# Kernel optimization log

Hardware: AMD Instinct MI355X
Metric: run time of the kernel (lower is better)

Reference implementation:

```python
import jax, jax.numpy as jnp
import numpy as np

N, E, D, K, NCONV = 50000, 800000, 64, 3, 6


def setup_inputs() -> dict:
    key = jax.random.key(0)
    ks = jax.random.split(key, 6)
    X = jax.random.normal(ks[0], (N, D), jnp.float32)
    edge_index = jax.random.randint(ks[1], (2, E), 0, N, dtype=jnp.int64)
    edge_weight = jax.random.uniform(ks[2], (E,), jnp.float32)
    H = jax.random.normal(ks[3], (N, D), jnp.float32)
    lambda_max = jnp.ones((1,), jnp.float32) * 2.0  # typical sym-normalized Laplacian bound
    conv_w = jax.random.normal(ks[4], (NCONV, K, D, D), jnp.float32) / np.sqrt(D)
    conv_b = jnp.zeros((NCONV, D), jnp.float32)
    return {"X": X, "edge_index": edge_index, "edge_weight": edge_weight,
            "H": H, "lambda_max": lambda_max, "conv_w": conv_w, "conv_b": conv_b}


def reference(X, edge_index, edge_weight, H, lambda_max, conv_w, conv_b):
    src, dst = edge_index[0], edge_index[1]
    # symmetric normalization: norm_e = w_e / sqrt(deg_src * deg_dst)
    deg = jax.ops.segment_sum(edge_weight, src, num_segments=N)
    dinv = jnp.where(deg > 0, deg ** -0.5, 0.0)
    norm = edge_weight * dinv[src] * dinv[dst]  # [E]
    lam = lambda_max.reshape(())
    c = 2.0 / lam

    def a_prop(v):  # A_norm @ v via scatter-add over edges, [N,D]
        return jax.ops.segment_sum(norm[:, None] * v[src], dst, num_segments=N)

    def l_hat(v):  # (2/lam)(I - A_norm) v - v
        return (c - 1.0) * v - c * a_prop(v)

    def cheb(v, w, b):  # ChebConv order K: sum_k T_k(L_hat) v @ W_k + b
        tx0, tx1 = v, l_hat(v)
        out = tx0 @ w[0] + tx1 @ w[1]
        for k in range(2, K):
            tx2 = 2.0 * l_hat(tx1) - tx0
            out = out + tx2 @ w[k]
            tx0, tx1 = tx1, tx2
        return out + b

    Z = jax.nn.sigmoid(cheb(X, conv_w[0], conv_b[0]) + cheb(H, conv_w[1], conv_b[1]))
    R = jax.nn.sigmoid(cheb(X, conv_w[2], conv_b[2]) + cheb(H, conv_w[3], conv_b[3]))
    H_tilde = jnp.tanh(cheb(X, conv_w[4], conv_b[4]) + cheb(H * R, conv_w[5], conv_b[5]))
    return Z * H_tilde + (1.0 - Z) * H
```

## Files before the change

kernel.cpp:

```cpp
#include <hip/hip_runtime.h>
#include <cstdint>
#include <cstddef>

typedef unsigned int u32;
typedef unsigned short u16;
typedef unsigned long long u64;

#define D 64
#define CAP 5120
#define CPAD 16
#define CEMAX 2048

typedef __attribute__((ext_vector_type(8))) short bf16x8;
typedef __attribute__((ext_vector_type(4))) float f32x4;

static __device__ __forceinline__ float sigmoidf_(float x) {
    return 1.f / (1.f + __expf(-x));
}
static __device__ __forceinline__ u16 f2bf(float x) {
    u32 u = __float_as_uint(x);
    return (u16)((u + 0x7fffu + ((u >> 16) & 1u)) >> 16);
}
static __device__ __forceinline__ u32 packbf2(float a, float b) {
    return (u32)f2bf(a) | ((u32)f2bf(b) << 16);
}
static __device__ __forceinline__ float bflo(u32 u) { return __uint_as_float(u << 16); }
static __device__ __forceinline__ float bfhi(u32 u) { return __uint_as_float(u & 0xffff0000u); }


__global__ void init_kernel(u32* cur_d, u32* cur_s) {
    int t = threadIdx.x;
    cur_d[t * CPAD] = (u32)(t * CAP);
    cur_s[t * CPAD] = (u32)(t * CAP);
}

__global__ __launch_bounds__(256) void coarse_prep_kernel(
    const int* __restrict__ src, const int* __restrict__ dst, const float* __restrict__ w,
    u32* cur_d, u32* cur_s,
    u64* __restrict__ slab_d, u32* __restrict__ slab_s,
    const float* __restrict__ X, const float* __restrict__ Hf,
    const float* __restrict__ convw,
    u32* __restrict__ XH_t, u32* __restrict__ WT,
    int E, int CE, int nch, int total) {
    __shared__ __align__(16) char smem[CEMAX * 12 + 6 * 1024];
    int t = threadIdx.x;
    int blk = blockIdx.x;

    if (blk >= nch) {
        int pb = blk - nch;
        if (pb < 18) {
            float (*s)[68] = (float (*)[68])smem;
            const float* wp = convw + (size_t)pb * 4096;
            for (int i = t; i < 1024; i += 256) {
                int k = i >> 4, c4 = (i & 15) * 4;
                *(float4*)&s[k][c4] = *(const float4*)&wp[k * 64 + c4];
            }
            __syncthreads();
            for (int i = t; i < 2048; i += 256) {
                int uk = i & 31, nn = i >> 5;
                WT[(size_t)pb * 2048 + nn * 32 + uk] = packbf2(s[2 * uk][nn], s[2 * uk + 1][nn]);
            }
            return;
        }
        int i = (pb - 18) * 256 + t;
        if (i >= total) return;
        int nn = i >> 6, l = i & 63;
        const float* sp = (l < 32 ? X : Hf) + (size_t)nn * 64 + ((2 * l) & 63);
        float2 v = *(const float2*)sp;
        XH_t[i] = packbf2(v.x, v.y);
        return;
    }

    u64* st_d = (u64*)smem;
    u32* st_s = (u32*)(smem + CEMAX * 8);
    u32* hd = (u32*)(smem + CEMAX * 12);
    u32* hs = hd + 256;
    u32* bd = hs + 256;
    u32* bs = bd + 256;
    u32* gd = bs + 256;
    u32* gs = gd + 256;
    int c = blk;
    hd[t] = 0; hs[t] = 0;
    __syncthreads();
    int e0 = c * CE, e1 = min(E, e0 + CE);
    int m = e1 - e0;
    for (int e = e0 + t; e < e1; e += 256) {
        atomicAdd(&hd[(u32)dst[e] >> 8], 1u);
        atomicAdd(&hs[(u32)src[e] >> 8], 1u);
    }
    __syncthreads();
    u32 vd = hd[t], vs = hs[t];
    bd[t] = vd; bs[t] = vs;
    __syncthreads();
    for (int o = 1; o < 256; o <<= 1) {
        u32 ad = (t >= o) ? bd[t - o] : 0u;
        u32 as = (t >= o) ? bs[t - o] : 0u;
        __syncthreads();
        bd[t] += ad; bs[t] += as;
        __syncthreads();
    }
    u32 exd = bd[t] - vd, exs = bs[t] - vs;
    gd[t] = atomicAdd(&cur_d[t * CPAD], vd);
    gs[t] = atomicAdd(&cur_s[t * CPAD], vs);
    bd[t] = exd; bs[t] = exs;
    hd[t] = exd; hs[t] = exs;
    __syncthreads();
    for (int e = e0 + t; e < e1; e += 256) {
        int s = src[e], d = dst[e];
        float wf = w[e];
        u32 pbd = (u32)d >> 8, pbs = (u32)s >> 8;
        u32 pd = atomicAdd(&hd[pbd], 1u);
        u32 ps = atomicAdd(&hs[pbs], 1u);
        st_d[pd] = (u64)((u32)s | (((u32)d & 255u) << 16) | (pbd << 24)) |
                   ((u64)__float_as_uint(wf) << 32);
        st_s[ps] = ((u32)s & 255u) | (pbs << 8) | ((u32)f2bf(wf) << 16);
    }
    __syncthreads();
    for (int i = t; i < m; i += 256) {
        u64 r = st_d[i];
        u32 b = (u32)(r >> 24) & 255u;
        u32 gpos = gd[b] + ((u32)i - bd[b]);
        if (gpos < (b + 1u) * CAP) slab_d[gpos] = r;
    }
    for (int i = t; i < m; i += 256) {
        u32 r = st_s[i];
        u32 b = (r >> 8) & 255u;
        u32 gpos = gs[b] + ((u32)i - bs[b]);
        if (gpos < (b + 1u) * CAP) slab_s[gpos] = r;
    }
}

__global__ __launch_bounds__(256) void fine_deg_bprefix_kernel(
    const u32* __restrict__ slab_s, const u32* __restrict__ cur_s,
    const u32* __restrict__ cur_d, float* __restrict__ dinv,
    u32* __restrict__ bstart, int NB, int N_) {
    int t = threadIdx.x;
    if ((int)blockIdx.x == NB) {
        __shared__ int sd[256];
        int v = (t < NB) ? min((int)cur_d[t * CPAD] - t * CAP, CAP) : 0;
        sd[t] = v;
        __syncthreads();
        for (int o = 1; o < 256; o <<= 1) {
            int a = (t >= o) ? sd[t - o] : 0;
            __syncthreads();
            sd[t] += a;
            __syncthreads();
        }
        bstart[t] = (u32)(sd[t] - v);
        return;
    }
    __shared__ float dg[256];
    int b = blockIdx.x;
    int m = min((int)cur_s[b * CPAD] - b * CAP, CAP);
    const u32* rp = slab_s + (size_t)b * CAP;
    dg[t] = 0.f;
    __syncthreads();
    for (int i = t; i < m; i += 256) {
        u32 r = rp[i];
        atomicAdd(&dg[r & 255u], __uint_as_float(r & 0xffff0000u));
    }
    __syncthreads();
    int node = (b << 8) + t;
    if (node < N_) dinv[node] = (dg[t] > 0.f) ? rsqrtf(dg[t]) : 0.f;
}

__global__ __launch_bounds__(256) void fine_dst_kernel(
    const u64* __restrict__ slab, const u32* __restrict__ cur_d,
    const u32* __restrict__ bstart, const float* __restrict__ dinv,
    u32* __restrict__ edge4,
    int* __restrict__ cnt, int* __restrict__ row_start, int N_) {
    __shared__ int h[256], sd[256], cur[256];
    int b = blockIdx.x, t = threadIdx.x;
    int m = min((int)cur_d[b * CPAD] - b * CAP, CAP);
    const u64* rp = slab + (size_t)b * CAP;
    h[t] = 0;
    __syncthreads();
    for (int i = t; i < m; i += 256) atomicAdd(&h[(int)((rp[i] >> 16) & 255u)], 1);
    __syncthreads();
    int v = h[t];
    sd[t] = v;
    __syncthreads();
    for (int o = 1; o < 256; o <<= 1) {
        int a = (t >= o) ? sd[t - o] : 0;
        __syncthreads();
        sd[t] += a;
        __syncthreads();
    }
    int excl = sd[t] - v;
    cur[t] = excl;
    int bs = (int)bstart[b];
    int node = (b << 8) + t;
    if (node < N_) { cnt[node] = v; row_start[node] = bs + excl; }
    __syncthreads();
    for (int i = t; i < m; i += 256) {
        u64 r = rp[i];
        int f = (int)((r >> 16) & 255u);
        int p = atomicAdd(&cur[f], 1);
        u32 sidx = (u32)(r & 0xffffu);
        float wf = __uint_as_float((u32)(r >> 32));
        float wn = wf * dinv[sidx];
        edge4[bs + p] = sidx | ((u32)f2bf(wn) << 16);
    }
}


__global__ __launch_bounds__(256) void lhat128_kernel(
    const u32* __restrict__ vt, const u32* __restrict__ w0t,
    u32* __restrict__ out_t,
    const int* __restrict__ rs, const int* __restrict__ cnt, const float* __restrict__ dinv,
    const u32* __restrict__ edges, const float* __restrict__ lam_ptr, int n) {
    int node = (blockIdx.x * blockDim.x + threadIdx.x) >> 6;
    if (node >= n) return;
    int l = threadIdx.x & 63;
    int g = l >> 4, f = l & 15;
    int e0 = rs[node], end = e0 + cnt[node];
    float acc[8];
#pragma unroll
    for (int j = 0; j < 8; j++) acc[j] = 0.f;

    int base = e0;
    for (; base + 16 <= end; base += 16) {
        u32 r0 = edges[base + g];
        u32 r1 = edges[base + 4 + g];
        u32 r2 = edges[base + 8 + g];
        u32 r3 = edges[base + 12 + g];
        const uint4 q0 = *(const uint4*)(vt + (size_t)(r0 & 0xffffu) * 64 + 4 * f);
        const uint4 q1 = *(const uint4*)(vt + (size_t)(r1 & 0xffffu) * 64 + 4 * f);
        const uint4 q2 = *(const uint4*)(vt + (size_t)(r2 & 0xffffu) * 64 + 4 * f);
        const uint4 q3 = *(const uint4*)(vt + (size_t)(r3 & 0xffffu) * 64 + 4 * f);
        float n0 = __uint_as_float(r0 & 0xffff0000u);
        float n1 = __uint_as_float(r1 & 0xffff0000u);
        float n2 = __uint_as_float(r2 & 0xffff0000u);
        float n3 = __uint_as_float(r3 & 0xffff0000u);
        acc[0] += n0 * bflo(q0.x); acc[1] += n0 * bfhi(q0.x);
        acc[2] += n0 * bflo(q0.y); acc[3] += n0 * bfhi(q0.y);
        acc[4] += n0 * bflo(q0.z); acc[5] += n0 * bfhi(q0.z);
        acc[6] += n0 * bflo(q0.w); acc[7] += n0 * bfhi(q0.w);
        acc[0] += n1 * bflo(q1.x); acc[1] += n1 * bfhi(q1.x);
        acc[2] += n1 * bflo(q1.y); acc[3] += n1 * bfhi(q1.y);
        acc[4] += n1 * bflo(q1.z); acc[5] += n1 * bfhi(q1.z);
        acc[6] += n1 * bflo(q1.w); acc[7] += n1 * bfhi(q1.w);
        acc[0] += n2 * bflo(q2.x); acc[1] += n2 * bfhi(q2.x);
        acc[2] += n2 * bflo(q2.y); acc[3] += n2 * bfhi(q2.y);
        acc[4] += n2 * bflo(q2.z); acc[5] += n2 * bfhi(q2.z);
        acc[6] += n2 * bflo(q2.w); acc[7] += n2 * bfhi(q2.w);
        acc[0] += n3 * bflo(q3.x); acc[1] += n3 * bfhi(q3.x);
        acc[2] += n3 * bflo(q3.y); acc[3] += n3 * bfhi(q3.y);
        acc[4] += n3 * bflo(q3.z); acc[5] += n3 * bfhi(q3.z);
        acc[6] += n3 * bflo(q3.w); acc[7] += n3 * bfhi(q3.w);
    }
    for (; base < end; base += 4) {
        int ei = base + g;
        u32 r0 = (ei < end) ? edges[ei] : 0u;
        const uint4 q0 = *(const uint4*)(vt + (size_t)(r0 & 0xffffu) * 64 + 4 * f);
        float n0 = __uint_as_float(r0 & 0xffff0000u);
        acc[0] += n0 * bflo(q0.x); acc[1] += n0 * bfhi(q0.x);
        acc[2] += n0 * bflo(q0.y); acc[3] += n0 * bfhi(q0.y);
        acc[4] += n0 * bflo(q0.z); acc[5] += n0 * bfhi(q0.z);
        acc[6] += n0 * bflo(q0.w); acc[7] += n0 * bfhi(q0.w);
    }
#pragma unroll
    for (int m = 16; m <= 32; m <<= 1)
#pragma unroll
        for (int j = 0; j < 8; j++) acc[j] += __shfl_xor(acc[j], m);

    const uint4 sv = *(const uint4*)(vt + (size_t)node * 64 + 4 * f);
    float self[8];
    self[0] = bflo(sv.x); self[1] = bfhi(sv.x);
    self[2] = bflo(sv.y); self[3] = bfhi(sv.y);
    self[4] = bflo(sv.z); self[5] = bfhi(sv.z);
    self[6] = bflo(sv.w); self[7] = bfhi(sv.w);
    float c = 2.f / lam_ptr[0];
    float dv = dinv[node];
    float rx[8];
#pragma unroll
    for (int j = 0; j < 8; j++) rx[j] = (c - 1.f) * self[j] - (c * dv) * acc[j];
    if (w0t) {
        const uint4 wv4 = *(const uint4*)(w0t + (size_t)node * 64 + 4 * f);
        rx[0] = 2.f * rx[0] - bflo(wv4.x); rx[1] = 2.f * rx[1] - bfhi(wv4.x);
        rx[2] = 2.f * rx[2] - bflo(wv4.y); rx[3] = 2.f * rx[3] - bfhi(wv4.y);
        rx[4] = 2.f * rx[4] - bflo(wv4.z); rx[5] = 2.f * rx[5] - bfhi(wv4.z);
        rx[6] = 2.f * rx[6] - bflo(wv4.w); rx[7] = 2.f * rx[7] - bfhi(wv4.w);
    }
    if (l < 16) {
        uint4 o;
        o.x = packbf2(rx[0], rx[1]); o.y = packbf2(rx[2], rx[3]);
        o.z = packbf2(rx[4], rx[5]); o.w = packbf2(rx[6], rx[7]);
        *(uint4*)(out_t + (size_t)node * 64 + 4 * f) = o;
    }
}

__global__ __launch_bounds__(256) void lhat64_kernel(
    const u32* __restrict__ vt, const u32* __restrict__ w0t,
    u32* __restrict__ out_t,
    const int* __restrict__ rs, const int* __restrict__ cnt, const float* __restrict__ dinv,
    const u32* __restrict__ edges, const float* __restrict__ lam_ptr, int n) {
    int node = (blockIdx.x * blockDim.x + threadIdx.x) >> 6;
    if (node >= n) return;
    int l = threadIdx.x & 63;
    int g = l >> 3, f = l & 7;
    int e0 = rs[node], end = e0 + cnt[node];
    float acc[8];
#pragma unroll
    for (int j = 0; j < 8; j++) acc[j] = 0.f;

    int base = e0;
    for (; base + 16 <= end; base += 16) {
        u32 r0 = edges[base + g];
        u32 r1 = edges[base + 8 + g];
        const uint4 q0 = *(const uint4*)(vt + (size_t)(r0 & 0xffffu) * 32 + 4 * f);
        const uint4 q1 = *(const uint4*)(vt + (size_t)(r1 & 0xffffu) * 32 + 4 * f);
        float n0 = __uint_as_float(r0 & 0xffff0000u);
        float n1 = __uint_as_float(r1 & 0xffff0000u);
        acc[0] += n0 * bflo(q0.x); acc[1] += n0 * bfhi(q0.x);
        acc[2] += n0 * bflo(q0.y); acc[3] += n0 * bfhi(q0.y);
        acc[4] += n0 * bflo(q0.z); acc[5] += n0 * bfhi(q0.z);
        acc[6] += n0 * bflo(q0.w); acc[7] += n0 * bfhi(q0.w);
        acc[0] += n1 * bflo(q1.x); acc[1] += n1 * bfhi(q1.x);
        acc[2] += n1 * bflo(q1.y); acc[3] += n1 * bfhi(q1.y);
        acc[4] += n1 * bflo(q1.z); acc[5] += n1 * bfhi(q1.z);
        acc[6] += n1 * bflo(q1.w); acc[7] += n1 * bfhi(q1.w);
    }
    for (; base < end; base += 8) {
        int ei = base + g;
        u32 r0 = (ei < end) ? edges[ei] : 0u;
        const uint4 q0 = *(const uint4*)(vt + (size_t)(r0 & 0xffffu) * 32 + 4 * f);
        float n0 = __uint_as_float(r0 & 0xffff0000u);
        acc[0] += n0 * bflo(q0.x); acc[1] += n0 * bfhi(q0.x);
        acc[2] += n0 * bflo(q0.y); acc[3] += n0 * bfhi(q0.y);
        acc[4] += n0 * bflo(q0.z); acc[5] += n0 * bfhi(q0.z);
        acc[6] += n0 * bflo(q0.w); acc[7] += n0 * bfhi(q0.w);
    }
#pragma unroll
    for (int m = 8; m <= 32; m <<= 1)
#pragma unroll
        for (int j = 0; j < 8; j++) acc[j] += __shfl_xor(acc[j], m);

    const uint4 sv = *(const uint4*)(vt + (size_t)node * 32 + 4 * f);
    float self[8];
    self[0] = bflo(sv.x); self[1] = bfhi(sv.x);
    self[2] = bflo(sv.y); self[3] = bfhi(sv.y);
    self[4] = bflo(sv.z); self[5] = bfhi(sv.z);
    self[6] = bflo(sv.w); self[7] = bfhi(sv.w);
    float c = 2.f / lam_ptr[0];
    float dv = dinv[node];
    float rx[8];
#pragma unroll
    for (int j = 0; j < 8; j++) rx[j] = (c - 1.f) * self[j] - (c * dv) * acc[j];
    if (w0t) {
        const uint4 wv4 = *(const uint4*)(w0t + (size_t)node * 32 + 4 * f);
        rx[0] = 2.f * rx[0] - bflo(wv4.x); rx[1] = 2.f * rx[1] - bfhi(wv4.x);
        rx[2] = 2.f * rx[2] - bflo(wv4.y); rx[3] = 2.f * rx[3] - bfhi(wv4.y);
        rx[4] = 2.f * rx[4] - bflo(wv4.z); rx[5] = 2.f * rx[5] - bfhi(wv4.z);
        rx[6] = 2.f * rx[6] - bflo(wv4.w); rx[7] = 2.f * rx[7] - bfhi(wv4.w);
    }
    if (l < 8) {
        uint4 o;
        o.x = packbf2(rx[0], rx[1]); o.y = packbf2(rx[2], rx[3]);
        o.z = packbf2(rx[4], rx[5]); o.w = packbf2(rx[6], rx[7]);
        *(uint4*)(out_t + (size_t)node * 32 + 4 * f) = o;
    }
}

__global__ __launch_bounds__(256) void gemm_gate_kernel(
    const u32* __restrict__ A0, const u32* __restrict__ A1, const u32* __restrict__ A2,
    const u32* __restrict__ WT, const float* __restrict__ convb,
    const float* __restrict__ Hf,
    float* __restrict__ Zb, float* __restrict__ Sh,
    u16* __restrict__ HR_t, int n) {
    __shared__ u32 Ws[64 * 36];
    int t = threadIdx.x;
    int wv = t >> 6, l = t & 63;
    int q = l >> 4, ml = l & 15;
    int R = blockIdx.x * 64 + wv * 16;
    int ar = R + ml; if (ar >= n) ar = n - 1;

    f32x4 S[3][4];
#pragma unroll
    for (int tg = 0; tg < 3; tg++)
#pragma unroll
        for (int ni = 0; ni < 4; ni++) S[tg][ni] = (f32x4){0.f, 0.f, 0.f, 0.f};

    for (int kt = 0; kt < 3; kt++) {
        const u32* Ap = (kt == 0) ? A0 : ((kt == 1) ? A1 : A2);
        const u32* ap = Ap + (size_t)ar * 64 + q * 4;
        bf16x8 af[2][2];
        af[0][0] = *(const bf16x8*)(ap +  0);
        af[1][0] = *(const bf16x8*)(ap + 16);
        af[0][1] = *(const bf16x8*)(ap + 32);
        af[1][1] = *(const bf16x8*)(ap + 48);
#pragma unroll
        for (int cg = 0; cg < 5; cg++) {
            int hf = cg & 1, tg = cg >> 1;
            const u32* Wp = WT + (size_t)(cg * 3 + kt) * 2048;
            __syncthreads();
            {
                int i0 = t * 4, i1 = i0 + 1024;
                uint4 w0 = *(const uint4*)(Wp + i0);
                uint4 w1 = *(const uint4*)(Wp + i1);
                *(uint4*)&Ws[(i0 >> 5) * 36 + (i0 & 31)] = w0;
                *(uint4*)&Ws[(i1 >> 5) * 36 + (i1 & 31)] = w1;
            }
            __syncthreads();
#pragma unroll
            for (int h = 0; h < 2; h++) {
                bf16x8 bw[4];
#pragma unroll
                for (int ni = 0; ni < 4; ni++)
                    bw[ni] = *(const bf16x8*)&Ws[(ni * 16 + ml) * 36 + q * 4 + h * 16];
#pragma unroll
                for (int ni = 0; ni < 4; ni++)
                    S[tg][ni] = __builtin_amdgcn_mfma_f32_16x16x32_bf16(
                        af[h][hf], bw[ni], S[tg][ni], 0, 0, 0);
            }
        }
    }
#pragma unroll
    for (int ni = 0; ni < 4; ni++) {
        int col = ni * 16 + ml;
        float bz = convb[col] + convb[64 + col];
        float br = convb[128 + col] + convb[192 + col];
#pragma unroll
        for (int reg = 0; reg < 4; reg++) {
            int row = R + q * 4 + reg;
            if (row < n) {
                size_t o = (size_t)row * 64 + col;
                float z = sigmoidf_(S[0][ni][reg] + bz);
                float r = sigmoidf_(S[1][ni][reg] + br);
                float hr = Hf[o] * r;
                Zb[o] = z;
                Sh[o] = S[2][ni][reg];
                HR_t[o] = f2bf(hr);
            }
        }
    }
}

__global__ __launch_bounds__(256) void gemm_final_kernel(
    const u32* __restrict__ A0, const u32* __restrict__ A1, const u32* __restrict__ A2,
    const u32* __restrict__ WT, const float* __restrict__ convb,
    const float* __restrict__ Zb, const float* __restrict__ Sh, const float* __restrict__ Hf,
    float* __restrict__ outp, int n) {
    __shared__ u32 Ws[64 * 36];
    int t = threadIdx.x;
    int wv = t >> 6, l = t & 63;
    int q = l >> 4, ml = l & 15;
    int R = blockIdx.x * 64 + wv * 16;
    int ar = R + ml; if (ar >= n) ar = n - 1;

    f32x4 S[4];
#pragma unroll
    for (int ni = 0; ni < 4; ni++) S[ni] = (f32x4){0.f, 0.f, 0.f, 0.f};

    for (int kt = 0; kt < 3; kt++) {
        const u32* Ap = (kt == 0) ? A0 : ((kt == 1) ? A1 : A2);
        const u32* ap = Ap + (size_t)ar * 32 + q * 4;
        bf16x8 af[2];
        af[0] = *(const bf16x8*)(ap +  0);
        af[1] = *(const bf16x8*)(ap + 16);
        const u32* Wp = WT + (size_t)(15 + kt) * 2048;
        __syncthreads();
        {
            int i0 = t * 4, i1 = i0 + 1024;
            uint4 w0 = *(const uint4*)(Wp + i0);
            uint4 w1 = *(const uint4*)(Wp + i1);
            *(uint4*)&Ws[(i0 >> 5) * 36 + (i0 & 31)] = w0;
            *(uint4*)&Ws[(i1 >> 5) * 36 + (i1 & 31)] = w1;
        }
        __syncthreads();
#pragma unroll
        for (int h = 0; h < 2; h++) {
            bf16x8 bw[4];
#pragma unroll
            for (int ni = 0; ni < 4; ni++)
                bw[ni] = *(const bf16x8*)&Ws[(ni * 16 + ml) * 36 + q * 4 + h * 16];
#pragma unroll
            for (int ni = 0; ni < 4; ni++)
                S[ni] = __builtin_amdgcn_mfma_f32_16x16x32_bf16(af[h], bw[ni], S[ni], 0, 0, 0);
        }
    }
#pragma unroll
    for (int ni = 0; ni < 4; ni++) {
        int col = ni * 16 + ml;
        float bh = convb[256 + col] + convb[320 + col];
#pragma unroll
        for (int reg = 0; reg < 4; reg++) {
            int row = R + q * 4 + reg;
            if (row < n) {
                size_t o = (size_t)row * 64 + col;
                float z = Zb[o];
                float ht = tanhf(S[ni][reg] + Sh[o] + bh);
                outp[o] = z * ht + (1.f - z) * Hf[o];
            }
        }
    }
}


extern "C" void kernel_launch(void* const* d_in, const int* in_sizes, int n_in,
                              void* d_out, int out_size, void* d_ws, size_t ws_size,
                              hipStream_t stream) {
    const float* X     = (const float*)d_in[0];
    const int*   ei    = (const int*)d_in[1];
    const float* ew    = (const float*)d_in[2];
    const float* H     = (const float*)d_in[3];
    const float* lam   = (const float*)d_in[4];
    const float* convw = (const float*)d_in[5];
    const float* convb = (const float*)d_in[6];
    float* out = (float*)d_out;

    const int N = in_sizes[0] / D;
    const int E = in_sizes[2];
    const int* src = ei;
    const int* dst = ei + E;

    const int NB = (N + 255) >> 8;
    const int nch = (E + CEMAX - 1) / CEMAX;
    const int CE = (E + nch - 1) / nch;

    char* p = (char*)d_ws;
    auto alloc = [&](size_t bytes) {
        void* r = (void*)p;
        p += (bytes + 255) & ~(size_t)255;
        return r;
    };
    float* Zb   = (float*)alloc((size_t)N * 64 * 4);
    float* Sh   = (float*)alloc((size_t)N * 64 * 4);
    u32* XH_t = (u32*)alloc((size_t)N * 64 * 4);
    u32* T1_t = (u32*)alloc((size_t)N * 64 * 4);
    u32* T2_t = (u32*)alloc((size_t)N * 64 * 4);
    u16* HR_t = (u16*)alloc((size_t)N * 64 * 2);
    u16* U1_t = (u16*)alloc((size_t)N * 64 * 2);
    u16* U2_t = (u16*)alloc((size_t)N * 64 * 2);
    u32* edge4 = (u32*)alloc((size_t)E * 4);
    u64* slab_d = (u64*)alloc((size_t)NB * CAP * 8);
    u32* slab_s = (u32*)alloc((size_t)NB * CAP * 4);
    u32* cur_d  = (u32*)alloc(256 * CPAD * 4);
    u32* cur_s  = (u32*)alloc(256 * CPAD * 4);
    u32* bstart = (u32*)alloc(256 * 4);
    int* cnt       = (int*)alloc((size_t)N * 4);
    int* row_start = (int*)alloc((size_t)N * 4);
    float* dinv    = (float*)alloc((size_t)N * 4);
    u32* WT = (u32*)alloc((size_t)18 * 2048 * 4);

    const int BLK = 256;
    const int gND  = (N * D + BLK - 1) / BLK;
    const int gWav = gND;
    const int gx64 = (N + 63) / 64;

    init_kernel<<<1, 256, 0, stream>>>(cur_d, cur_s);
    coarse_prep_kernel<<<nch + 18 + gND, BLK, 0, stream>>>(
        src, dst, ew, cur_d, cur_s, slab_d, slab_s,
        X, H, convw, XH_t, WT, E, CE, nch, N * D);
    fine_deg_bprefix_kernel<<<NB + 1, BLK, 0, stream>>>(slab_s, cur_s, cur_d, dinv, bstart, NB, N);
    fine_dst_kernel<<<NB, BLK, 0, stream>>>(slab_d, cur_d, bstart, dinv, edge4, cnt, row_start, N);

    lhat128_kernel<<<gWav, BLK, 0, stream>>>(XH_t, nullptr, T1_t,
                                             row_start, cnt, dinv, edge4, lam, N);
    lhat128_kernel<<<gWav, BLK, 0, stream>>>(T1_t, XH_t, T2_t,
                                             row_start, cnt, dinv, edge4, lam, N);

    gemm_gate_kernel<<<gx64, BLK, 0, stream>>>(XH_t, T1_t, T2_t, WT, convb, H,
                                               Zb, Sh, HR_t, N);

    lhat64_kernel<<<gWav, BLK, 0, stream>>>((const u32*)HR_t, nullptr, (u32*)U1_t,
                                            row_start, cnt, dinv, edge4, lam, N);
    lhat64_kernel<<<gWav, BLK, 0, stream>>>((const u32*)U1_t, (const u32*)HR_t, (u32*)U2_t,
                                            row_start, cnt, dinv, edge4, lam, N);

    gemm_final_kernel<<<gx64, BLK, 0, stream>>>((const u32*)HR_t, (const u32*)U1_t, (const u32*)U2_t,
                                                WT, convb, Zb, Sh, H, out, N);
}
```

Baseline: 286.8 us.

## Merge fine binning kernels, apply source dinv in SpMM, widen GEMM blocks

```diff
diff --git a/kernel.cpp b/kernel.cpp
--- a/kernel.cpp
+++ b/kernel.cpp
@@ -130,49 +130,32 @@
     }
 }
 
-__global__ __launch_bounds__(256) void fine_deg_bprefix_kernel(
-    const u32* __restrict__ slab_s, const u32* __restrict__ cur_s,
-    const u32* __restrict__ cur_d, float* __restrict__ dinv,
-    u32* __restrict__ bstart, int NB, int N_) {
+__global__ __launch_bounds__(256) void fine_fused_kernel(
+    const u64* __restrict__ slab_d, const u32* __restrict__ slab_s,
+    const u32* __restrict__ cur_d, const u32* __restrict__ cur_s,
+    float* __restrict__ dinv, u32* __restrict__ edge4,
+    int* __restrict__ cnt, int* __restrict__ row_start, int NB, int N_) {
     int t = threadIdx.x;
-    if ((int)blockIdx.x == NB) {
-        __shared__ int sd[256];
-        int v = (t < NB) ? min((int)cur_d[t * CPAD] - t * CAP, CAP) : 0;
-        sd[t] = v;
-        __syncthreads();
-        for (int o = 1; o < 256; o <<= 1) {
-            int a = (t >= o) ? sd[t - o] : 0;
-            __syncthreads();
-            sd[t] += a;
-            __syncthreads();
-        }
-        bstart[t] = (u32)(sd[t] - v);
+    int b = blockIdx.x;
+    if (b < NB) {
+        __shared__ float dg[256];
+        int m = min((int)cur_s[b * CPAD] - b * CAP, CAP);
+        const u32* rp = slab_s + (size_t)b * CAP;
+        dg[t] = 0.f;
+        __syncthreads();
+        for (int i = t; i < m; i += 256) {
+            u32 r = rp[i];
+            atomicAdd(&dg[r & 255u], __uint_as_float(r & 0xffff0000u));
+        }
+        __syncthreads();
+        int node = (b << 8) + t;
+        if (node < N_) dinv[node] = (dg[t] > 0.f) ? rsqrtf(dg[t]) : 0.f;
         return;
     }
-    __shared__ float dg[256];
-    int b = blockIdx.x;
-    int m = min((int)cur_s[b * CPAD] - b * CAP, CAP);
-    const u32* rp = slab_s + (size_t)b * CAP;
-    dg[t] = 0.f;
-    __syncthreads();
-    for (int i = t; i < m; i += 256) {
-        u32 r = rp[i];
-        atomicAdd(&dg[r & 255u], __uint_as_float(r & 0xffff0000u));
-    }
-    __syncthreads();
-    int node = (b << 8) + t;
-    if (node < N_) dinv[node] = (dg[t] > 0.f) ? rsqrtf(dg[t]) : 0.f;
-}
-
-__global__ __launch_bounds__(256) void fine_dst_kernel(
-    const u64* __restrict__ slab, const u32* __restrict__ cur_d,
-    const u32* __restrict__ bstart, const float* __restrict__ dinv,
-    u32* __restrict__ edge4,
-    int* __restrict__ cnt, int* __restrict__ row_start, int N_) {
+    b -= NB;
     __shared__ int h[256], sd[256], cur[256];
-    int b = blockIdx.x, t = threadIdx.x;
     int m = min((int)cur_d[b * CPAD] - b * CAP, CAP);
-    const u64* rp = slab + (size_t)b * CAP;
+    const u64* rp = slab_d + (size_t)b * CAP;
     h[t] = 0;
     __syncthreads();
     for (int i = t; i < m; i += 256) atomicAdd(&h[(int)((rp[i] >> 16) & 255u)], 1);
@@ -188,7 +171,7 @@
     }
     int excl = sd[t] - v;
     cur[t] = excl;
-    int bs = (int)bstart[b];
+    int bs = b * CAP;
     int node = (b << 8) + t;
     if (node < N_) { cnt[node] = v; row_start[node] = bs + excl; }
     __syncthreads();
@@ -198,8 +181,7 @@
         int p = atomicAdd(&cur[f], 1);
         u32 sidx = (u32)(r & 0xffffu);
         float wf = __uint_as_float((u32)(r >> 32));
-        float wn = wf * dinv[sidx];
-        edge4[bs + p] = sidx | ((u32)f2bf(wn) << 16);
+        edge4[bs + p] = sidx | ((u32)f2bf(wf) << 16);
     }
 }
 
@@ -224,14 +206,18 @@
         u32 r1 = edges[base + 4 + g];
         u32 r2 = edges[base + 8 + g];
         u32 r3 = edges[base + 12 + g];
+        float d0 = dinv[r0 & 0xffffu];
+        float d1 = dinv[r1 & 0xffffu];
+        float d2 = dinv[r2 & 0xffffu];
+        float d3 = dinv[r3 & 0xffffu];
         const uint4 q0 = *(const uint4*)(vt + (size_t)(r0 & 0xffffu) * 64 + 4 * f);
         const uint4 q1 = *(const uint4*)(vt + (size_t)(r1 & 0xffffu) * 64 + 4 * f);
         const uint4 q2 = *(const uint4*)(vt + (size_t)(r2 & 0xffffu) * 64 + 4 * f);
         const uint4 q3 = *(const uint4*)(vt + (size_t)(r3 & 0xffffu) * 64 + 4 * f);
-        float n0 = __uint_as_float(r0 & 0xffff0000u);
-        float n1 = __uint_as_float(r1 & 0xffff0000u);
-        float n2 = __uint_as_float(r2 & 0xffff0000u);
-        float n3 = __uint_as_float(r3 & 0xffff0000u);
+        float n0 = __uint_as_float(r0 & 0xffff0000u) * d0;
+        float n1 = __uint_as_float(r1 & 0xffff0000u) * d1;
+        float n2 = __uint_as_float(r2 & 0xffff0000u) * d2;
+        float n3 = __uint_as_float(r3 & 0xffff0000u) * d3;
         acc[0] += n0 * bflo(q0.x); acc[1] += n0 * bfhi(q0.x);
         acc[2] += n0 * bflo(q0.y); acc[3] += n0 * bfhi(q0.y);
         acc[4] += n0 * bflo(q0.z); acc[5] += n0 * bfhi(q0.z);
@@ -252,8 +238,9 @@
     for (; base < end; base += 4) {
         int ei = base + g;
         u32 r0 = (ei < end) ? edges[ei] : 0u;
+        float d0 = dinv[r0 & 0xffffu];
         const uint4 q0 = *(const uint4*)(vt + (size_t)(r0 & 0xffffu) * 64 + 4 * f);
-        float n0 = __uint_as_float(r0 & 0xffff0000u);
+        float n0 = __uint_as_float(r0 & 0xffff0000u) * d0;
         acc[0] += n0 * bflo(q0.x); acc[1] += n0 * bfhi(q0.x);
         acc[2] += n0 * bflo(q0.y); acc[3] += n0 * bfhi(q0.y);
         acc[4] += n0 * bflo(q0.z); acc[5] += n0 * bfhi(q0.z);
@@ -308,10 +295,12 @@
     for (; base + 16 <= end; base += 16) {
         u32 r0 = edges[base + g];
         u32 r1 = edges[base + 8 + g];
+        float d0 = dinv[r0 & 0xffffu];
+        float d1 = dinv[r1 & 0xffffu];
         const uint4 q0 = *(const uint4*)(vt + (size_t)(r0 & 0xffffu) * 32 + 4 * f);
         const uint4 q1 = *(const uint4*)(vt + (size_t)(r1 & 0xffffu) * 32 + 4 * f);
-        float n0 = __uint_as_float(r0 & 0xffff0000u);
-        float n1 = __uint_as_float(r1 & 0xffff0000u);
+        float n0 = __uint_as_float(r0 & 0xffff0000u) * d0;
+        float n1 = __uint_as_float(r1 & 0xffff0000u) * d1;
         acc[0] += n0 * bflo(q0.x); acc[1] += n0 * bfhi(q0.x);
         acc[2] += n0 * bflo(q0.y); acc[3] += n0 * bfhi(q0.y);
         acc[4] += n0 * bflo(q0.z); acc[5] += n0 * bfhi(q0.z);
@@ -324,8 +313,9 @@
     for (; base < end; base += 8) {
         int ei = base + g;
         u32 r0 = (ei < end) ? edges[ei] : 0u;
+        float d0 = dinv[r0 & 0xffffu];
         const uint4 q0 = *(const uint4*)(vt + (size_t)(r0 & 0xffffu) * 32 + 4 * f);
-        float n0 = __uint_as_float(r0 & 0xffff0000u);
+        float n0 = __uint_as_float(r0 & 0xffff0000u) * d0;
         acc[0] += n0 * bflo(q0.x); acc[1] += n0 * bfhi(q0.x);
         acc[2] += n0 * bflo(q0.y); acc[3] += n0 * bfhi(q0.y);
         acc[4] += n0 * bflo(q0.z); acc[5] += n0 * bfhi(q0.z);
@@ -362,7 +352,7 @@
     }
 }
 
-__global__ __launch_bounds__(256) void gemm_gate_kernel(
+__global__ __launch_bounds__(512) void gemm_gate_kernel(
     const u32* __restrict__ A0, const u32* __restrict__ A1, const u32* __restrict__ A2,
     const u32* __restrict__ WT, const float* __restrict__ convb,
     const float* __restrict__ Hf,
@@ -372,7 +362,7 @@
     int t = threadIdx.x;
     int wv = t >> 6, l = t & 63;
     int q = l >> 4, ml = l & 15;
-    int R = blockIdx.x * 64 + wv * 16;
+    int R = blockIdx.x * 128 + wv * 16;
     int ar = R + ml; if (ar >= n) ar = n - 1;
 
     f32x4 S[3][4];
@@ -395,11 +385,9 @@
             const u32* Wp = WT + (size_t)(cg * 3 + kt) * 2048;
             __syncthreads();
             {
-                int i0 = t * 4, i1 = i0 + 1024;
+                int i0 = t * 4;
                 uint4 w0 = *(const uint4*)(Wp + i0);
-                uint4 w1 = *(const uint4*)(Wp + i1);
                 *(uint4*)&Ws[(i0 >> 5) * 36 + (i0 & 31)] = w0;
-                *(uint4*)&Ws[(i1 >> 5) * 36 + (i1 & 31)] = w1;
             }
             __syncthreads();
 #pragma unroll
@@ -436,7 +424,7 @@
     }
 }
 
-__global__ __launch_bounds__(256) void gemm_final_kernel(
+__global__ __launch_bounds__(512) void gemm_final_kernel(
     const u32* __restrict__ A0, const u32* __restrict__ A1, const u32* __restrict__ A2,
     const u32* __restrict__ WT, const float* __restrict__ convb,
     const float* __restrict__ Zb, const float* __restrict__ Sh, const float* __restrict__ Hf,
@@ -445,7 +433,7 @@
     int t = threadIdx.x;
     int wv = t >> 6, l = t & 63;
     int q = l >> 4, ml = l & 15;
-    int R = blockIdx.x * 64 + wv * 16;
+    int R = blockIdx.x * 128 + wv * 16;
     int ar = R + ml; if (ar >= n) ar = n - 1;
 
     f32x4 S[4];
@@ -461,11 +449,9 @@
         const u32* Wp = WT + (size_t)(15 + kt) * 2048;
         __syncthreads();
         {
-            int i0 = t * 4, i1 = i0 + 1024;
+            int i0 = t * 4;
             uint4 w0 = *(const uint4*)(Wp + i0);
-            uint4 w1 = *(const uint4*)(Wp + i1);
             *(uint4*)&Ws[(i0 >> 5) * 36 + (i0 & 31)] = w0;
-            *(uint4*)&Ws[(i1 >> 5) * 36 + (i1 & 31)] = w1;
         }
         __syncthreads();
 #pragma unroll
@@ -532,12 +518,11 @@
     u16* HR_t = (u16*)alloc((size_t)N * 64 * 2);
     u16* U1_t = (u16*)alloc((size_t)N * 64 * 2);
     u16* U2_t = (u16*)alloc((size_t)N * 64 * 2);
-    u32* edge4 = (u32*)alloc((size_t)E * 4);
+    u32* edge4 = (u32*)alloc((size_t)NB * CAP * 4);
     u64* slab_d = (u64*)alloc((size_t)NB * CAP * 8);
     u32* slab_s = (u32*)alloc((size_t)NB * CAP * 4);
     u32* cur_d  = (u32*)alloc(256 * CPAD * 4);
     u32* cur_s  = (u32*)alloc(256 * CPAD * 4);
-    u32* bstart = (u32*)alloc(256 * 4);
     int* cnt       = (int*)alloc((size_t)N * 4);
     int* row_start = (int*)alloc((size_t)N * 4);
     float* dinv    = (float*)alloc((size_t)N * 4);
@@ -546,28 +531,28 @@
     const int BLK = 256;
     const int gND  = (N * D + BLK - 1) / BLK;
     const int gWav = gND;
-    const int gx64 = (N + 63) / 64;
+    const int gx128 = (N + 127) / 128;
 
     init_kernel<<<1, 256, 0, stream>>>(cur_d, cur_s);
     coarse_prep_kernel<<<nch + 18 + gND, BLK, 0, stream>>>(
         src, dst, ew, cur_d, cur_s, slab_d, slab_s,
         X, H, convw, XH_t, WT, E, CE, nch, N * D);
-    fine_deg_bprefix_kernel<<<NB + 1, BLK, 0, stream>>>(slab_s, cur_s, cur_d, dinv, bstart, NB, N);
-    fine_dst_kernel<<<NB, BLK, 0, stream>>>(slab_d, cur_d, bstart, dinv, edge4, cnt, row_start, N);
+    fine_fused_kernel<<<2 * NB, BLK, 0, stream>>>(slab_d, slab_s, cur_d, cur_s,
+                                                  dinv, edge4, cnt, row_start, NB, N);
 
     lhat128_kernel<<<gWav, BLK, 0, stream>>>(XH_t, nullptr, T1_t,
                                              row_start, cnt, dinv, edge4, lam, N);
     lhat128_kernel<<<gWav, BLK, 0, stream>>>(T1_t, XH_t, T2_t,
                                              row_start, cnt, dinv, edge4, lam, N);
 
-    gemm_gate_kernel<<<gx64, BLK, 0, stream>>>(XH_t, T1_t, T2_t, WT, convb, H,
-                                               Zb, Sh, HR_t, N);
+    gemm_gate_kernel<<<gx128, 512, 0, stream>>>(XH_t, T1_t, T2_t, WT, convb, H,
+                                                Zb, Sh, HR_t, N);
 
     lhat64_kernel<<<gWav, BLK, 0, stream>>>((const u32*)HR_t, nullptr, (u32*)U1_t,
                                             row_start, cnt, dinv, edge4, lam, N);
     lhat64_kernel<<<gWav, BLK, 0, stream>>>((const u32*)U1_t, (const u32*)HR_t, (u32*)U2_t,
                                             row_start, cnt, dinv, edge4, lam, N);
 
-    gemm_final_kernel<<<gx64, BLK, 0, stream>>>((const u32*)HR_t, (const u32*)U1_t, (const u32*)U2_t,
-                                                WT, convb, Zb, Sh, H, out, N);
-}
+    gemm_final_kernel<<<gx128, 512, 0, stream>>>((const u32*)HR_t, (const u32*)U1_t, (const u32*)U2_t,
+                                                 WT, convb, Zb, Sh, H, out, N);
+}
```

After: 282.7 us. About the same (-1.4%).
